# Kernel optimization log

Measured on AMD Instinct MI355X. Metric: run time of the kernel, lower is better.

## Reference

```python
import jax, jax.numpy as jnp
import numpy as np

FEATURE_DIM = 256
NUM_HEADS = 4
HEAD_DIM = FEATURE_DIM // NUM_HEADS  # 64
B, N = 4, 2048


def _conv1x1(x, w, b):
    # x: [B, C_in, N], w: [C_out, C_in], b: [C_out] -> [B, C_out, N]
    return jnp.einsum('oc,bcn->bon', w, x) + b[None, :, None]


def setup_inputs() -> dict:
    key = jax.random.key(0)
    ks = jax.random.split(key, 11)
    std = 0.02
    d = {
        'query': jax.random.normal(ks[0], (B, FEATURE_DIM, N), jnp.float32),
        'key': jax.random.normal(ks[1], (B, FEATURE_DIM, N), jnp.float32),
        'value': jax.random.normal(ks[2], (B, FEATURE_DIM, N), jnp.float32),
        'wq': jax.random.normal(ks[3], (FEATURE_DIM, FEATURE_DIM), jnp.float32) * std,
        'bq': jnp.zeros((FEATURE_DIM,), jnp.float32),
        'wk': jax.random.normal(ks[4], (FEATURE_DIM, FEATURE_DIM), jnp.float32) * std,
        'bk': jnp.zeros((FEATURE_DIM,), jnp.float32),
        'wv': jax.random.normal(ks[5], (FEATURE_DIM, FEATURE_DIM), jnp.float32) * std,
        'bv': jnp.zeros((FEATURE_DIM,), jnp.float32),
        'wm': jax.random.normal(ks[6], (FEATURE_DIM, FEATURE_DIM), jnp.float32) * std,
        'bm': jnp.zeros((FEATURE_DIM,), jnp.float32),
    }
    return d


def reference(query, key, value, wq, bq, wk, bk, wv, bv, wm, bm):
    b = query.shape[0]
    # 1x1 conv projections, then split channels as (head_dim, num_heads) -- head_dim outer,
    # matching torch's .view(b, head_dim, num_heads, -1)
    q = _conv1x1(query, wq, bq).reshape(b, HEAD_DIM, NUM_HEADS, -1)
    k = _conv1x1(key, wk, bk).reshape(b, HEAD_DIM, NUM_HEADS, -1)
    v = _conv1x1(value, wv, bv).reshape(b, HEAD_DIM, NUM_HEADS, -1)
    scores = jnp.einsum('bdhn,bdhm->bhnm', q, k) / jnp.sqrt(jnp.asarray(HEAD_DIM, q.dtype))
    probs = jax.nn.softmax(scores, axis=-1)
    out = jnp.einsum('bhnm,bdhm->bdhn', probs, v)
    out = out.reshape(b, HEAD_DIM * NUM_HEADS, -1)
    return _conv1x1(out, wm, bm)
```

## Files before the change

kernel.cpp:

```cpp
#include <hip/hip_runtime.h>
#include <math.h>

#define B_ 4
#define C_ 256
#define N_ 2048
#define H_ 4
#define D_ 64

typedef __attribute__((ext_vector_type(8))) short bf16x8;
typedef __attribute__((ext_vector_type(4))) float f32x4;

#define QSCALE 0.18033688011112042f

__device__ __forceinline__ float fexp2(float x) {
#if __has_builtin(__builtin_amdgcn_exp2f)
    return __builtin_amdgcn_exp2f(x);
#else
    float r;
    asm("v_exp_f32 %0, %1\n\ts_nop 1" : "=v"(r) : "v"(x));
    return r;
#endif
}

__device__ __forceinline__ ushort f2bf(float x) {
    uint u = __float_as_uint(x);
    uint r = (u + 0x7fffu + ((u >> 16) & 1u)) >> 16;
    return (ushort)r;
}
__device__ __forceinline__ float bf2f(ushort u) {
    return __uint_as_float((uint)u << 16);
}
__device__ __forceinline__ uint4 pack8(const ushort* v) {
    uint4 r;
    r.x = (uint)v[0] | ((uint)v[1] << 16);
    r.y = (uint)v[2] | ((uint)v[3] << 16);
    r.z = (uint)v[4] | ((uint)v[5] << 16);
    r.w = (uint)v[6] | ((uint)v[7] << 16);
    return r;
}
__device__ __forceinline__ void glds16(const void* g, void* l) {
    __builtin_amdgcn_global_load_lds(
        (const __attribute__((address_space(1))) unsigned int*)g,
        (__attribute__((address_space(3))) unsigned int*)l, 16, 0, 0);
}

__global__ __launch_bounds__(256) void pack_w(const float* __restrict__ w0,
                                              const float* __restrict__ w1,
                                              const float* __restrict__ w2,
                                              const float* __restrict__ w3,
                                              ushort* __restrict__ Whimg,
                                              ushort* __restrict__ Wlimg) {
    const int ws = blockIdx.x;
    const int ks = blockIdx.y;
    const float* W = ws == 0 ? w0 : ws == 1 ? w1 : ws == 2 ? w2 : w3;
    ushort* Hh = Whimg + ws * 65536;
    ushort* Hl = Wlimg + ws * 65536;
    const int o  = threadIdx.x;
    const int of = o >> 4;
    const int li = o & 15;

    float v[32];
#pragma unroll
    for (int q = 0; q < 8; ++q)
        *(float4*)&v[q * 4] = *(const float4*)&W[o * 256 + ks * 32 + q * 4];

#pragma unroll
    for (int g = 0; g < 4; ++g) {
        ushort hi[8], lo[8];
#pragma unroll
        for (int e = 0; e < 8; ++e) {
            const float x = v[g * 8 + e];
            hi[e] = f2bf(x);
            lo[e] = f2bf(x - bf2f(hi[e]));
        }
        const size_t dst = ((size_t)(ks * 16 + of) * 64 + (g * 16 + li)) * 8;
        *(uint4*)(Hh + dst) = pack8(hi);
        if (ws == 3) *(uint4*)(Hl + dst) = pack8(lo);
    }
}

__global__ __launch_bounds__(256) void proj_fused(const float* __restrict__ Xq,
                                                  const float* __restrict__ Xk,
                                                  const float* __restrict__ Xv,
                                                  const ushort* __restrict__ Whimg,
                                                  const float* __restrict__ bq,
                                                  const float* __restrict__ bk,
                                                  const float* __restrict__ bv,
                                                  ushort* __restrict__ Qb,
                                                  ushort* __restrict__ Kimg,
                                                  ushort* __restrict__ Vimg) {
    __shared__ float  Xf[2][2048];
    __shared__ ushort Xb[2][2048];
    __shared__ ushort Ls[32][264];

    const int z   = blockIdx.z;
    const int sel = z >> 2, b = z & 3;
    const int nt  = blockIdx.x;
    const int n0  = nt * 32;
    const int tid  = threadIdx.x;
    const int wv   = tid >> 6;
    const int lane = tid & 63;
    const int li   = lane & 15;
    const int g    = lane >> 4;
    const int l7   = li & 7;

    const float* X = (sel == 0 ? Xq : sel == 1 ? Xk : Xv) + (size_t)b * C_ * N_;
    const ushort* Wh  = Whimg + sel * 65536;
    const float* bias = sel == 0 ? bq : sel == 1 ? bk : bv;

    const int st_row = wv * 16 + (lane >> 3);
    const int st_col = (lane & 7) * 4;

    const int cv_n  = tid & 31;
    const int cv_g  = tid >> 5;
    const int cv_c0 = cv_g * 8;
    const int cv_sl = (cv_g ^ (cv_n & 7)) * 8;

#define PSTAGE(buf, s_)                                                          \
    do {                                                                         \
        const float* p_ = X + (size_t)((s_) * 64 + st_row) * N_ + n0 + st_col;   \
        glds16(p_,          &Xf[buf][wv * 512]);                                 \
        glds16(p_ + 8 * N_, &Xf[buf][wv * 512 + 256]);                           \
    } while (0)

#define PCONV(dst, src)                                                          \
    do {                                                                         \
        ushort t_[8];                                                            \
        _Pragma("unroll")                                                        \
        for (int e = 0; e < 8; ++e)                                              \
            t_[e] = f2bf(Xf[src][(cv_c0 + e) * 32 + cv_n]);                      \
        *(uint4*)&Xb[dst][cv_n * 64 + cv_sl] = pack8(t_);                        \
    } while (0)

    PSTAGE(0, 0);
    __syncthreads();
    PSTAGE(1, 1);
    PCONV(0, 0);
    __syncthreads();

    const f32x4 zv = {0.f, 0.f, 0.f, 0.f};
    f32x4 acc[4][2] = {{zv, zv}, {zv, zv}, {zv, zv}, {zv, zv}};

    for (int st = 0; st < 4; ++st) {
        if (st + 2 < 4) PSTAGE(st & 1, st + 2);
        if (st + 1 < 4) PCONV((st + 1) & 1, (st + 1) & 1);

        bf16x8 xb[2][2];
#pragma unroll
        for (int nf = 0; nf < 2; ++nf)
#pragma unroll
            for (int ksub = 0; ksub < 2; ++ksub)
                xb[nf][ksub] = *(const bf16x8*)
                    &Xb[st & 1][(16 * nf + li) * 64 + 8 * (((ksub << 2) + g) ^ l7)];

        __builtin_amdgcn_s_setprio(1);
#pragma unroll
        for (int ksub = 0; ksub < 2; ++ksub) {
            const size_t ab = ((size_t)((2 * st + ksub) * 16 + wv * 4) * 64 + lane) * 8;
#pragma unroll
            for (int ot = 0; ot < 4; ++ot) {
                const bf16x8 ah = *(const bf16x8*)(Wh + ab + (size_t)ot * 512);
#pragma unroll
                for (int nf = 0; nf < 2; ++nf)
                    acc[ot][nf] = __builtin_amdgcn_mfma_f32_16x16x32_bf16(
                        ah, xb[nf][ksub], acc[ot][nf], 0, 0, 0);
            }
        }
        __builtin_amdgcn_s_setprio(0);
        __syncthreads();
    }

    const float scale = (sel == 0) ? QSCALE : 1.0f;
#pragma unroll
    for (int ot = 0; ot < 4; ++ot)
#pragma unroll
        for (int nf = 0; nf < 2; ++nf)
#pragma unroll
            for (int r = 0; r < 4; ++r) {
                const int o = wv * 64 + ot * 16 + g * 4 + r;
                Ls[nf * 16 + li][o] = f2bf((acc[ot][nf][r] + bias[o]) * scale);
            }
    __syncthreads();

    const int h  = tid >> 6;
    const int bh = b * 4 + h;
    if (sel == 0) {
#pragma unroll
        for (int r_ = 0; r_ < 4; ++r_) {
            const int gi = (tid & 63) + 64 * r_;
            const int n_l = gi >> 3, dr = gi & 7;
            ushort u[8];
#pragma unroll
            for (int e = 0; e < 8; ++e) u[e] = Ls[n_l][(dr * 8 + e) * 4 + h];
            *(uint4*)(Qb + (((size_t)bh * N_) + n0 + n_l) * 64 + dr * 8) = pack8(u);
        }
    } else if (sel == 1) {
#pragma unroll
        for (int r_ = 0; r_ < 4; ++r_) {
            const int gi = (tid & 63) + 64 * r_;
            const int n_l = gi >> 3, dr = gi & 7;
            ushort u[8];
#pragma unroll
            for (int e = 0; e < 8; ++e) u[e] = Ls[n_l][(dr * 8 + e) * 4 + h];
            const int jg    = n0 + n_l;
            const int j     = jg & 63;
            const int ktile = jg >> 6;
            *(uint4*)(Kimg + (((size_t)bh * 32 + ktile) << 12) + j * 64 +
                      ((dr * 8) ^ ((j & 7) << 3))) = pack8(u);
        }
    } else {
#pragma unroll
        for (int r_ = 0; r_ < 4; ++r_) {
            const int gi = (tid & 63) + 64 * r_;
            const int d = gi >> 2, jr = gi & 3;
            ushort u[8];
#pragma unroll
            for (int e = 0; e < 8; ++e) u[e] = Ls[jr * 8 + e][d * 4 + h];
            const int jbase = (nt & 1) * 32 + jr * 8;
            const int ktile = nt >> 1;
            *(uint4*)(Vimg + (((size_t)bh * 32 + ktile) << 12) + d * 64 +
                      (jbase ^ ((d & 7) << 3))) = pack8(u);
        }
    }
#undef PSTAGE
#undef PCONV
}

__global__ __launch_bounds__(256) void attn_v7(const ushort* __restrict__ Qb,
                                               const ushort* __restrict__ Kimg,
                                               const ushort* __restrict__ Vimg,
                                               float* __restrict__ Opart,
                                               float* __restrict__ lpart) {
    __shared__ ushort SMEM[24576];

    const int bid = blockIdx.x;
    const int L   = (bid & 7) * 64 + (bid >> 3);
    const int qt  = L & 15;
    const int ps  = L >> 4;
    const int bh  = ps >> 1;
    const int s   = ps & 1;

    const int tid  = threadIdx.x;
    const int wv   = tid >> 6;
    const int lane = tid & 63;
    const int li   = lane & 15;
    const int g    = lane >> 4;
    const int l7   = li & 7;
    const int i0w  = qt * 128 + wv * 32;

    bf16x8 qf[2][2];
#pragma unroll
    for (int qg = 0; qg < 2; ++qg)
#pragma unroll
        for (int ks = 0; ks < 2; ++ks)
            qf[qg][ks] = *(const bf16x8*)(Qb + ((size_t)bh * N_ + i0w + qg * 16 + li) * 64 +
                                          ks * 32 + g * 8);

    const ushort* Kg = Kimg + ((size_t)bh << 17);
    const ushort* Vg = Vimg + ((size_t)bh << 17);
    ushort* Pw = SMEM + 16384 + wv * 2048;

    const f32x4 z = {0.f, 0.f, 0.f, 0.f};
    f32x4 accO[4][2] = {{z, z}, {z, z}, {z, z}, {z, z}};
    f32x4 accL[2] = {z, z};
    const bf16x8 ones = {16256, 16256, 16256, 16256, 16256, 16256, 16256, 16256};

    const int kt0 = s * 16, kt1 = kt0 + 16;

#define STAGE(buf, kt_)                                                          \
    do {                                                                         \
        const ushort* ksrc = Kg + ((size_t)(kt_) << 12) + wv * 1024 + lane * 8;  \
        const ushort* vsrc = Vg + ((size_t)(kt_) << 12) + wv * 1024 + lane * 8;  \
        glds16(ksrc,       SMEM + (buf) * 4096 + wv * 1024);                     \
        glds16(ksrc + 512, SMEM + (buf) * 4096 + wv * 1024 + 512);               \
        glds16(vsrc,       SMEM + 8192 + (buf) * 4096 + wv * 1024);              \
        glds16(vsrc + 512, SMEM + 8192 + (buf) * 4096 + wv * 1024 + 512);        \
    } while (0)

    STAGE(0, kt0);
    __syncthreads();

    int cur = 0;
    for (int kt = kt0; kt < kt1; ++kt) {
        if (kt + 1 < kt1) STAGE(cur ^ 1, kt + 1);

        const ushort* Kc = SMEM + cur * 4096;
        const ushort* Vc = SMEM + 8192 + cur * 4096;

        f32x4 sc[4][2];
        __builtin_amdgcn_s_setprio(1);
#pragma unroll
        for (int jt = 0; jt < 4; ++jt) {
            const ushort* row = Kc + (16 * jt + li) * 64;
            const bf16x8 kf0 = *(const bf16x8*)(row + 8 * (g ^ l7));
            const bf16x8 kf1 = *(const bf16x8*)(row + 8 * ((4 + g) ^ l7));
#pragma unroll
            for (int qg = 0; qg < 2; ++qg) {
                f32x4 a = z;
                a = __builtin_amdgcn_mfma_f32_16x16x32_bf16(kf0, qf[qg][0], a, 0, 0, 0);
                a = __builtin_amdgcn_mfma_f32_16x16x32_bf16(kf1, qf[qg][1], a, 0, 0, 0);
                sc[jt][qg] = a;
            }
        }
        __builtin_amdgcn_s_setprio(0);

#pragma unroll
        for (int qg = 0; qg < 2; ++qg) {
            const uint rowb = (uint)((qg * 16 + li) * 128);
#pragma unroll
            for (int jt = 0; jt < 4; ++jt) {
                const float p0 = fexp2(sc[jt][qg][0]);
                const float p1 = fexp2(sc[jt][qg][1]);
                const float p2 = fexp2(sc[jt][qg][2]);
                const float p3 = fexp2(sc[jt][qg][3]);
                const uint a01 = (__float_as_uint(p1) & 0xffff0000u) | (__float_as_uint(p0) >> 16);
                const uint a23 = (__float_as_uint(p3) & 0xffff0000u) | (__float_as_uint(p2) >> 16);
                const uint byteoff = rowb + (((uint)(jt * 32 + g * 8)) ^ ((uint)l7 << 4));
                *(uint2*)((char*)Pw + byteoff) = make_uint2(a01, a23);
            }
        }

        bf16x8 pf[2][2];
#pragma unroll
        for (int qg = 0; qg < 2; ++qg)
#pragma unroll
            for (int ks = 0; ks < 2; ++ks)
                pf[qg][ks] = *(const bf16x8*)((char*)Pw + (qg * 16 + li) * 128 +
                                              16 * ((4 * ks + g) ^ l7));

        __builtin_amdgcn_s_setprio(1);
#pragma unroll
        for (int qg = 0; qg < 2; ++qg) {
            accL[qg] = __builtin_amdgcn_mfma_f32_16x16x32_bf16(ones, pf[qg][0], accL[qg], 0, 0, 0);
            accL[qg] = __builtin_amdgcn_mfma_f32_16x16x32_bf16(ones, pf[qg][1], accL[qg], 0, 0, 0);
        }

#pragma unroll
        for (int dt = 0; dt < 4; ++dt) {
            const ushort* row = Vc + (16 * dt + li) * 64;
            const bf16x8 vf0 = *(const bf16x8*)(row + 8 * (g ^ l7));
            const bf16x8 vf1 = *(const bf16x8*)(row + 8 * ((4 + g) ^ l7));
#pragma unroll
            for (int qg = 0; qg < 2; ++qg) {
                f32x4 a = accO[dt][qg];
                a = __builtin_amdgcn_mfma_f32_16x16x32_bf16(vf0, pf[qg][0], a, 0, 0, 0);
                a = __builtin_amdgcn_mfma_f32_16x16x32_bf16(vf1, pf[qg][1], a, 0, 0, 0);
                accO[dt][qg] = a;
            }
        }
        __builtin_amdgcn_s_setprio(0);

        __syncthreads();
        cur ^= 1;
    }
#undef STAGE

    const int sbase = (s * 16 + bh) * 128 + qt * 8 + wv * 2;
#pragma unroll
    for (int qg = 0; qg < 2; ++qg) {
        const int slot = sbase + qg;
        float* Op = Opart + (size_t)slot * 1024;
#pragma unroll
        for (int dt = 0; dt < 4; ++dt)
            *(f32x4*)&Op[li * 64 + dt * 16 + g * 4] = accO[dt][qg];
        if (g == 0) lpart[slot * 16 + li] = accL[qg][0];
    }
}

__global__ __launch_bounds__(256) void conv_out(const float* __restrict__ Opart,
                                                const float* __restrict__ lpart,
                                                const ushort* __restrict__ Whimg,
                                                const ushort* __restrict__ Wlimg,
                                                const float* __restrict__ bm,
                                                float* __restrict__ out) {
    __shared__ ushort Bh[512 * 8];
    __shared__ ushort Bl[512 * 8];
    __shared__ float Linv[4][16];

    const int bx  = blockIdx.x;
    const int b   = blockIdx.y;
    const int n0  = bx * 16;
    const int qt  = bx >> 2;
    const int wq  = bx & 3;
    const int tid = threadIdx.x;

    if (tid < 64) {
        const int h = tid >> 4, q = tid & 15;
        const int sl0 = (((0 * 16 + b * 4 + h) * 32 + qt) * 4 + wq);
        const int sl1 = (((1 * 16 + b * 4 + h) * 32 + qt) * 4 + wq);
        Linv[h][q] = 1.0f / (lpart[sl0 * 16 + q] + lpart[sl1 * 16 + q]);
    }
    __syncthreads();

#pragma unroll
    for (int it = 0; it < 4; ++it) {
        const int id = tid + 256 * it;
        const int h  = id >> 8;
        const int q  = (id >> 4) & 15;
        const int d4 = id & 15;
        const size_t sl0 = (size_t)(((0 * 16 + b * 4 + h) * 32 + qt) * 4 + wq);
        const size_t sl1 = (size_t)(((1 * 16 + b * 4 + h) * 32 + qt) * 4 + wq);
        const f32x4 v0 = *(const f32x4*)&Opart[sl0 * 1024 + q * 64 + d4 * 4];
        const f32x4 v1 = *(const f32x4*)&Opart[sl1 * 1024 + q * 64 + d4 * 4];
        const float li_ = Linv[h][q];
#pragma unroll
        for (int e = 0; e < 4; ++e) {
            const int d = d4 * 4 + e;
            const float vv = (v0[e] + v1[e]) * li_;
            const ushort hi = f2bf(vv);
            const ushort lo = f2bf(vv - bf2f(hi));
            const int cg = d >> 1;
            const int eb = (d & 1) * 4 + h;
            const int Gp = (q * 32 + cg) ^ (q & 7);
            Bh[Gp * 8 + eb] = hi;
            Bl[Gp * 8 + eb] = lo;
        }
    }
    __syncthreads();

    const int wv = tid >> 6, lane = tid & 63, li = lane & 15, g = lane >> 4;
    const ushort* Wh = Whimg + 3 * 65536;
    const ushort* Wl = Wlimg + 3 * 65536;
    const f32x4 zv = {0.f, 0.f, 0.f, 0.f};
    f32x4 acc[4] = {zv, zv, zv, zv};

    for (int ks = 0; ks < 8; ++ks) {
        const int Gp = (li * 32 + ks * 4 + g) ^ (li & 7);
        const bf16x8 bh_ = *(const bf16x8*)(Bh + Gp * 8);
        const bf16x8 bl_ = *(const bf16x8*)(Bl + Gp * 8);
        const size_t abase = ((size_t)(ks * 16 + wv * 4) * 64 + lane) * 8;
#pragma unroll
        for (int ot = 0; ot < 4; ++ot) {
            const bf16x8 ah = *(const bf16x8*)(Wh + abase + (size_t)ot * 512);
            const bf16x8 al = *(const bf16x8*)(Wl + abase + (size_t)ot * 512);
            f32x4 a = acc[ot];
            a = __builtin_amdgcn_mfma_f32_16x16x32_bf16(ah, bl_, a, 0, 0, 0);
            a = __builtin_amdgcn_mfma_f32_16x16x32_bf16(al, bh_, a, 0, 0, 0);
            a = __builtin_amdgcn_mfma_f32_16x16x32_bf16(ah, bh_, a, 0, 0, 0);
            acc[ot] = a;
        }
    }

#pragma unroll
    for (int ot = 0; ot < 4; ++ot)
#pragma unroll
        for (int r = 0; r < 4; ++r) {
            const int o = wv * 64 + ot * 16 + g * 4 + r;
            out[((size_t)(b * 256 + o)) * N_ + n0 + li] = acc[ot][r] + bm[o];
        }
}

extern "C" void kernel_launch(void* const* d_in, const int* in_sizes, int n_in,
                              void* d_out, int out_size, void* d_ws, size_t ws_size,
                              hipStream_t stream) {
    const float* query = (const float*)d_in[0];
    const float* key   = (const float*)d_in[1];
    const float* value = (const float*)d_in[2];
    const float* wq = (const float*)d_in[3];
    const float* bq = (const float*)d_in[4];
    const float* wk = (const float*)d_in[5];
    const float* bk = (const float*)d_in[6];
    const float* wv = (const float*)d_in[7];
    const float* bv = (const float*)d_in[8];
    const float* wm = (const float*)d_in[9];
    const float* bm = (const float*)d_in[10];

    float* out = (float*)d_out;
    char*  ws  = (char*)d_ws;

    const size_t TEN = (size_t)B_ * C_ * N_;

    float*  Opart = (float*)ws;
    float*  lpart = (float*)(ws + (size_t)4096 * 1024 * 4);
    ushort* Qb    = (ushort*)(ws + (size_t)4096 * 1024 * 4 + 262144);
    ushort* Kimg  = Qb + TEN;
    ushort* Vimg  = Kimg + TEN;
    ushort* Whimg = Vimg + TEN;
    ushort* Wlimg = Whimg + 4 * 65536;

    pack_w<<<dim3(4, 8), dim3(256), 0, stream>>>(wq, wk, wv, wm, Whimg, Wlimg);
    proj_fused<<<dim3(64, 1, 12), dim3(256), 0, stream>>>(query, key, value,
                                                          Whimg, bq, bk, bv,
                                                          Qb, Kimg, Vimg);
    attn_v7<<<dim3(512), dim3(256), 0, stream>>>(Qb, Kimg, Vimg, Opart, lpart);
    conv_out<<<dim3(128, 4), dim3(256), 0, stream>>>(Opart, lpart, Whimg, Wlimg, bm, out);
}
```

Measured before the change: 61.58 us.

## Retile output projection to 64 columns per block with output-channel split

The output 1x1 conv kernel now processes 64 sequence positions per block instead of 16, with 512 threads and the 256 output channels split across two blocks in z. Each wave loads one weight fragment per k-step and reuses it across four column fragments, rather than loading four weight fragments and reusing one B fragment. This cuts global weight traffic per output and writes wider contiguous rows, at the cost of more LDS per block, fewer blocks (256 instead of 512), and recomputing the normalized attention tile twice, once per output-channel half.

```diff
diff --git a/kernel.cpp b/kernel.cpp
--- a/kernel.cpp
+++ b/kernel.cpp
@@ -367,46 +367,52 @@
     }
 }
 
-__global__ __launch_bounds__(256) void conv_out(const float* __restrict__ Opart,
+__global__ __launch_bounds__(512) void conv_out(const float* __restrict__ Opart,
                                                 const float* __restrict__ lpart,
                                                 const ushort* __restrict__ Whimg,
                                                 const ushort* __restrict__ Wlimg,
                                                 const float* __restrict__ bm,
                                                 float* __restrict__ out) {
-    __shared__ ushort Bh[512 * 8];
-    __shared__ ushort Bl[512 * 8];
-    __shared__ float Linv[4][16];
+    __shared__ ushort Bh[2048 * 8];
+    __shared__ ushort Bl[2048 * 8];
+    __shared__ float Linv[4][64];
 
     const int bx  = blockIdx.x;
     const int b   = blockIdx.y;
-    const int n0  = bx * 16;
-    const int qt  = bx >> 2;
-    const int wq  = bx & 3;
+    const int oh  = blockIdx.z;
+    const int n0  = bx * 64;
     const int tid = threadIdx.x;
 
-    if (tid < 64) {
-        const int h = tid >> 4, q = tid & 15;
-        const int sl0 = (((0 * 16 + b * 4 + h) * 32 + qt) * 4 + wq);
-        const int sl1 = (((1 * 16 + b * 4 + h) * 32 + qt) * 4 + wq);
-        Linv[h][q] = 1.0f / (lpart[sl0 * 16 + q] + lpart[sl1 * 16 + q]);
+    if (tid < 256) {
+        const int h = tid >> 6, q = tid & 63;
+        const int gq = (n0 + q) >> 4;
+        const int qi = q & 15;
+        const int sl0 = (0 * 16 + b * 4 + h) * 128 + gq;
+        const int sl1 = (1 * 16 + b * 4 + h) * 128 + gq;
+        Linv[h][q] = 1.0f / (lpart[sl0 * 16 + qi] + lpart[sl1 * 16 + qi]);
     }
     __syncthreads();
 
 #pragma unroll
     for (int it = 0; it < 4; ++it) {
-        const int id = tid + 256 * it;
-        const int h  = id >> 8;
-        const int q  = (id >> 4) & 15;
-        const int d4 = id & 15;
-        const size_t sl0 = (size_t)(((0 * 16 + b * 4 + h) * 32 + qt) * 4 + wq);
-        const size_t sl1 = (size_t)(((1 * 16 + b * 4 + h) * 32 + qt) * 4 + wq);
-        const f32x4 v0 = *(const f32x4*)&Opart[sl0 * 1024 + q * 64 + d4 * 4];
-        const f32x4 v1 = *(const f32x4*)&Opart[sl1 * 1024 + q * 64 + d4 * 4];
+        const int id = tid + 512 * it;
+        const int h  = id >> 9;
+        const int q  = (id >> 3) & 63;
+        const int d0 = (id & 7) * 8;
+        const int gq = (n0 + q) >> 4;
+        const int qi = q & 15;
+        const size_t sl0 = (size_t)((0 * 16 + b * 4 + h) * 128 + gq);
+        const size_t sl1 = (size_t)((1 * 16 + b * 4 + h) * 128 + gq);
+        const f32x4 v0a = *(const f32x4*)&Opart[sl0 * 1024 + qi * 64 + d0];
+        const f32x4 v0b = *(const f32x4*)&Opart[sl0 * 1024 + qi * 64 + d0 + 4];
+        const f32x4 v1a = *(const f32x4*)&Opart[sl1 * 1024 + qi * 64 + d0];
+        const f32x4 v1b = *(const f32x4*)&Opart[sl1 * 1024 + qi * 64 + d0 + 4];
         const float li_ = Linv[h][q];
 #pragma unroll
-        for (int e = 0; e < 4; ++e) {
-            const int d = d4 * 4 + e;
-            const float vv = (v0[e] + v1[e]) * li_;
+        for (int e = 0; e < 8; ++e) {
+            const int d = d0 + e;
+            const float vv = ((e < 4 ? v0a[e & 3] : v0b[e & 3]) +
+                              (e < 4 ? v1a[e & 3] : v1b[e & 3])) * li_;
             const ushort hi = f2bf(vv);
             const ushort lo = f2bf(vv - bf2f(hi));
             const int cg = d >> 1;
@@ -419,34 +425,35 @@
     __syncthreads();
 
     const int wv = tid >> 6, lane = tid & 63, li = lane & 15, g = lane >> 4;
+    const int of = oh * 8 + wv;
     const ushort* Wh = Whimg + 3 * 65536;
     const ushort* Wl = Wlimg + 3 * 65536;
     const f32x4 zv = {0.f, 0.f, 0.f, 0.f};
     f32x4 acc[4] = {zv, zv, zv, zv};
 
     for (int ks = 0; ks < 8; ++ks) {
-        const int Gp = (li * 32 + ks * 4 + g) ^ (li & 7);
-        const bf16x8 bh_ = *(const bf16x8*)(Bh + Gp * 8);
-        const bf16x8 bl_ = *(const bf16x8*)(Bl + Gp * 8);
-        const size_t abase = ((size_t)(ks * 16 + wv * 4) * 64 + lane) * 8;
-#pragma unroll
-        for (int ot = 0; ot < 4; ++ot) {
-            const bf16x8 ah = *(const bf16x8*)(Wh + abase + (size_t)ot * 512);
-            const bf16x8 al = *(const bf16x8*)(Wl + abase + (size_t)ot * 512);
-            f32x4 a = acc[ot];
+        const size_t abase = ((size_t)(ks * 16 + of) * 64 + lane) * 8;
+        const bf16x8 ah = *(const bf16x8*)(Wh + abase);
+        const bf16x8 al = *(const bf16x8*)(Wl + abase);
+#pragma unroll
+        for (int nf = 0; nf < 4; ++nf) {
+            const int Gp = ((16 * nf + li) * 32 + ks * 4 + g) ^ (li & 7);
+            const bf16x8 bh_ = *(const bf16x8*)(Bh + Gp * 8);
+            const bf16x8 bl_ = *(const bf16x8*)(Bl + Gp * 8);
+            f32x4 a = acc[nf];
             a = __builtin_amdgcn_mfma_f32_16x16x32_bf16(ah, bl_, a, 0, 0, 0);
             a = __builtin_amdgcn_mfma_f32_16x16x32_bf16(al, bh_, a, 0, 0, 0);
             a = __builtin_amdgcn_mfma_f32_16x16x32_bf16(ah, bh_, a, 0, 0, 0);
-            acc[ot] = a;
-        }
-    }
-
-#pragma unroll
-    for (int ot = 0; ot < 4; ++ot)
+            acc[nf] = a;
+        }
+    }
+
+#pragma unroll
+    for (int nf = 0; nf < 4; ++nf)
 #pragma unroll
         for (int r = 0; r < 4; ++r) {
-            const int o = wv * 64 + ot * 16 + g * 4 + r;
-            out[((size_t)(b * 256 + o)) * N_ + n0 + li] = acc[ot][r] + bm[o];
+            const int o = oh * 128 + wv * 16 + g * 4 + r;
+            out[((size_t)(b * 256 + o)) * N_ + n0 + nf * 16 + li] = acc[nf][r] + bm[o];
         }
 }
 
@@ -483,5 +490,5 @@
                                                           Whimg, bq, bk, bv,
                                                           Qb, Kimg, Vimg);
     attn_v7<<<dim3(512), dim3(256), 0, stream>>>(Qb, Kimg, Vimg, Opart, lpart);
-    conv_out<<<dim3(128, 4), dim3(256), 0, stream>>>(Opart, lpart, Whimg, Wlimg, bm, out);
-}
+    conv_out<<<dim3(32, 4, 2), dim3(512), 0, stream>>>(Opart, lpart, Whimg, Wlimg, bm, out);
+}
```

After: 59.42 us. 1.04x faster.
